# Kernel tuning notes

Hardware: AMD Instinct MI355X
Metric: run time of the kernel (lower is better)

Reference implementation:

```python
import jax, jax.numpy as jnp
import numpy as np

N_EMBED = 1024
HEAD_COUNT = 16
HEAD_SIZE = 64  # HEAD_COUNT * HEAD_SIZE == N_EMBED
SEQ = 2048
BATCH = 2


def setup_inputs() -> dict:
    key = jax.random.key(0)
    k_ix, k_q, k_k, k_v, k_p, k_b = jax.random.split(key, 6)
    scale = 1.0 / np.sqrt(N_EMBED)
    inp = {
        "ix": jax.random.normal(k_ix, (BATCH, SEQ, N_EMBED), dtype=jnp.float32),
        # per-head projection weights, stored as x @ W form: [H, C, D]
        "Wq": jax.random.normal(k_q, (HEAD_COUNT, N_EMBED, HEAD_SIZE), dtype=jnp.float32) * scale,
        "Wk": jax.random.normal(k_k, (HEAD_COUNT, N_EMBED, HEAD_SIZE), dtype=jnp.float32) * scale,
        "Wv": jax.random.normal(k_v, (HEAD_COUNT, N_EMBED, HEAD_SIZE), dtype=jnp.float32) * scale,
        # output projection (Linear with bias): y = x @ Wp + bp
        "Wp": jax.random.normal(k_p, (N_EMBED, N_EMBED), dtype=jnp.float32) * scale,
        "bp": jax.random.normal(k_b, (N_EMBED,), dtype=jnp.float32) * scale,
    }
    return inp


def reference(ix, Wq, Wk, Wv, Wp, bp):
    B, T, C = ix.shape
    # per-head projections: [B, H, T, D]
    Q = jnp.einsum("btc,hcd->bhtd", ix, Wq)
    K = jnp.einsum("btc,hcd->bhtd", ix, Wk)
    V = jnp.einsum("btc,hcd->bhtd", ix, Wv)
    # NOTE: faithful to source -- scores are MULTIPLIED by sqrt(C) (C = n_embed)
    scores = jnp.einsum("bhtd,bhsd->bhts", Q, K) * (C ** 0.5)
    causal = jnp.tril(jnp.ones((T, T), dtype=bool))
    scores = jnp.where(causal, scores, -jnp.inf)
    wei = jax.nn.softmax(scores, axis=-1)
    out = jnp.einsum("bhts,bhsd->bhtd", wei, V)
    # concat heads (matches torch.cat over per-head outputs along last dim)
    out = out.transpose(0, 2, 1, 3).reshape(B, T, -1)
    return out @ Wp + bp
```

## Files before the change

### kernel.cpp

```cpp
#include <hip/hip_runtime.h>

#define BATCH 2
#define SEQL  2048
#define NEMB  1024
#define NH    16
#define HD    64
#define MROWS (BATCH*SEQL)

typedef short bf16x8 __attribute__((ext_vector_type(8)));
typedef float f32x16 __attribute__((ext_vector_type(16)));

__device__ __forceinline__ unsigned short f2bf(float x) {
    union { float f; unsigned u; } v; v.f = x;
    unsigned r = v.u + 0x7FFFu + ((v.u >> 16) & 1u);
    return (unsigned short)(r >> 16);
}
__device__ __forceinline__ void split_bf16(float x, unsigned short& hi, unsigned short& lo) {
    hi = f2bf(x);
    union { unsigned u; float f; } h; h.u = ((unsigned)hi) << 16;
    lo = f2bf(x - h.f);
}

__device__ __forceinline__ int slot16(int chunk, int lane) {
    return chunk * 66 + (lane & 31) + 33 * (lane >> 5);
}

__global__ __launch_bounds__(256) void split_convert_kernel(
    const float* __restrict__ src,
    unsigned short* __restrict__ dhi, unsigned short* __restrict__ dlo)
{
    int i = (blockIdx.x * 256 + threadIdx.x) * 4;
    float4 v = *(const float4*)(src + i);
    unsigned short h[4], l[4];
    split_bf16(v.x, h[0], l[0]); split_bf16(v.y, h[1], l[1]);
    split_bf16(v.z, h[2], l[2]); split_bf16(v.w, h[3], l[3]);
    uint2 ph, pl;
    ph.x = h[0] | ((unsigned)h[1] << 16); ph.y = h[2] | ((unsigned)h[3] << 16);
    pl.x = l[0] | ((unsigned)l[1] << 16); pl.y = l[2] | ((unsigned)l[3] << 16);
    *(uint2*)(dhi + i) = ph;
    *(uint2*)(dlo + i) = pl;
}

__global__ __launch_bounds__(256) void transpose_convert_kernel(
    const float* __restrict__ Wq, const float* __restrict__ Wk,
    const float* __restrict__ Wv, const float* __restrict__ Wp,
    unsigned short* __restrict__ qhi, unsigned short* __restrict__ qlo,
    unsigned short* __restrict__ khi, unsigned short* __restrict__ klo,
    unsigned short* __restrict__ vhi, unsigned short* __restrict__ pt)
{
    __shared__ float tile[64][68];
    const int z = blockIdx.z, hb = blockIdx.y, c0 = blockIdx.x * 64;
    const float* src; int rstride; unsigned short* dhi; unsigned short* dlo;
    if (z == 0)      { src = Wq + (size_t)hb * 65536; rstride = 64;   dhi = qhi; dlo = qlo; }
    else if (z == 1) { src = Wk + (size_t)hb * 65536; rstride = 64;   dhi = khi; dlo = klo; }
    else if (z == 2) { src = Wv + (size_t)hb * 65536; rstride = 64;   dhi = vhi; dlo = nullptr; }
    else             { src = Wp + (size_t)hb * 64;    rstride = 1024; dhi = pt;  dlo = nullptr; }
    const int tid = threadIdx.x;
    #pragma unroll
    for (int i = 0; i < 4; ++i) {
        int fidx = i * 256 + tid;
        int r  = fidx >> 4;
        int dq = (fidx & 15) * 4;
        float4 v = *(const float4*)(src + (size_t)(c0 + r) * rstride + dq);
        *(float4*)&tile[r][dq] = v;
    }
    __syncthreads();
    #pragma unroll
    for (int i = 0; i < 4; ++i) {
        int fidx = i * 256 + tid;
        int d  = fidx >> 4;
        int cq = (fidx & 15) * 4;
        size_t base = (size_t)(hb * 64 + d) * 1024 + c0 + cq;
        unsigned short hh[4], ll[4];
        #pragma unroll
        for (int j = 0; j < 4; ++j) split_bf16(tile[cq + j][d], hh[j], ll[j]);
        uint2 ph; ph.x = hh[0] | ((unsigned)hh[1] << 16); ph.y = hh[2] | ((unsigned)hh[3] << 16);
        *(uint2*)(dhi + base) = ph;
        if (dlo) {
            uint2 pl; pl.x = ll[0] | ((unsigned)ll[1] << 16); pl.y = ll[2] | ((unsigned)ll[3] << 16);
            *(uint2*)(dlo + base) = pl;
        }
    }
}

__global__ __launch_bounds__(256) void qkv_gemm(
    const unsigned short* __restrict__ Ahi, const unsigned short* __restrict__ Alo,
    const unsigned short* __restrict__ Bq_hi, const unsigned short* __restrict__ Bq_lo,
    const unsigned short* __restrict__ Bk_hi, const unsigned short* __restrict__ Bk_lo,
    const unsigned short* __restrict__ Bv_hi,
    unsigned short* __restrict__ Qhi, unsigned short* __restrict__ Qlo,
    unsigned short* __restrict__ Khi, unsigned short* __restrict__ Klo,
    unsigned short* __restrict__ Vt)
{
    __shared__ unsigned short smem[16896];
    unsigned short* a_hi = smem;
    unsigned short* b_hi = smem + 4224;

    const int z = blockIdx.z;
    const bool split = (z < 2);
    const unsigned short* __restrict__ Bhi = (z == 0) ? Bq_hi : (z == 1) ? Bk_hi : Bv_hi;
    const unsigned short* __restrict__ Blo = (z == 0) ? Bq_lo : Bk_lo;
    unsigned short* __restrict__ Ohi = (z == 0) ? Qhi : Khi;
    unsigned short* __restrict__ Olo = (z == 0) ? Qlo : Klo;
    const float oscale = (z == 0) ? 32.0f : 1.0f;

    const int m0 = blockIdx.x * 128;
    const int n0 = blockIdx.y * 128;
    const int tid  = threadIdx.x;
    const int wid  = tid >> 6, lane = tid & 63;
    const int wr   = wid >> 1, wc = wid & 1;

    f32x16 acc[2][2] = {};

    for (int kk0 = 0; kk0 < NEMB; kk0 += 32) {
        __syncthreads();
        #pragma unroll
        for (int q = 0; q < 2; ++q) {
            int fidx = q * 256 + tid;
            int row  = fidx >> 2;
            int k8   = (fidx & 3) * 8;
            int chunk = (row >> 5) * 2 + (k8 >> 4);
            int lp    = (row & 31) + 32 * ((k8 >> 3) & 1);
            int slot  = slot16(chunk, lp) * 8;
            *(bf16x8*)(a_hi + slot) = *(const bf16x8*)(Ahi + (size_t)(m0 + row) * 1024 + kk0 + k8);
            *(bf16x8*)(b_hi + slot) = *(const bf16x8*)(Bhi + (size_t)(n0 + row) * 1024 + kk0 + k8);
            if (split) {
                *(bf16x8*)(smem + 8448  + slot) = *(const bf16x8*)(Alo + (size_t)(m0 + row) * 1024 + kk0 + k8);
                *(bf16x8*)(smem + 12672 + slot) = *(const bf16x8*)(Blo + (size_t)(n0 + row) * 1024 + kk0 + k8);
            }
        }
        __syncthreads();
        #pragma unroll
        for (int kch = 0; kch < 2; ++kch) {
            bf16x8 ah[2], bh_[2];
            #pragma unroll
            for (int mt = 0; mt < 2; ++mt)
                ah[mt] = *(const bf16x8*)(a_hi + slot16((2 * wr + mt) * 2 + kch, lane) * 8);
            #pragma unroll
            for (int nt = 0; nt < 2; ++nt)
                bh_[nt] = *(const bf16x8*)(b_hi + slot16((2 * wc + nt) * 2 + kch, lane) * 8);
            if (split) {
                bf16x8 al[2], bl[2];
                #pragma unroll
                for (int mt = 0; mt < 2; ++mt)
                    al[mt] = *(const bf16x8*)(smem + 8448 + slot16((2 * wr + mt) * 2 + kch, lane) * 8);
                #pragma unroll
                for (int nt = 0; nt < 2; ++nt)
                    bl[nt] = *(const bf16x8*)(smem + 12672 + slot16((2 * wc + nt) * 2 + kch, lane) * 8);
                #pragma unroll
                for (int mt = 0; mt < 2; ++mt)
                    #pragma unroll
                    for (int nt = 0; nt < 2; ++nt) {
                        acc[mt][nt] = __builtin_amdgcn_mfma_f32_32x32x16_bf16(ah[mt], bh_[nt], acc[mt][nt], 0, 0, 0);
                        acc[mt][nt] = __builtin_amdgcn_mfma_f32_32x32x16_bf16(ah[mt], bl[nt],  acc[mt][nt], 0, 0, 0);
                        acc[mt][nt] = __builtin_amdgcn_mfma_f32_32x32x16_bf16(al[mt], bh_[nt], acc[mt][nt], 0, 0, 0);
                    }
            } else {
                #pragma unroll
                for (int mt = 0; mt < 2; ++mt)
                    #pragma unroll
                    for (int nt = 0; nt < 2; ++nt)
                        acc[mt][nt] = __builtin_amdgcn_mfma_f32_32x32x16_bf16(bh_[nt], ah[mt], acc[mt][nt], 0, 0, 0);
            }
        }
    }

    #pragma unroll
    for (int mt = 0; mt < 2; ++mt) {
        #pragma unroll
        for (int nt = 0; nt < 2; ++nt) {
            if (z == 2) {
                const int mcol = m0 + wr * 64 + mt * 32 + (lane & 31);
                const int bb = mcol >> 11, tt = mcol & (SEQL - 1);
                #pragma unroll
                for (int r = 0; r < 16; ++r) {
                    int nrow = n0 + wc * 64 + nt * 32 + (r & 3) + 8 * (r >> 2) + 4 * (lane >> 5);
                    int head = nrow >> 6, dd = nrow & 63;
                    Vt[((size_t)(bb * NH + head) * HD + dd) * SEQL + tt] = f2bf(acc[mt][nt][r]);
                }
            } else {
                const int ncol = n0 + wc * 64 + nt * 32 + (lane & 31);
                const int head = ncol >> 6, d = ncol & 63;
                #pragma unroll
                for (int r = 0; r < 16; ++r) {
                    int mrow = m0 + wr * 64 + mt * 32 + (r & 3) + 8 * (r >> 2) + 4 * (lane >> 5);
                    int bb = mrow >> 11, t = mrow & (SEQL - 1);
                    size_t idx = ((size_t)(bb * NH + head) * SEQL + t) * HD + d;
                    float v = acc[mt][nt][r] * oscale;
                    unsigned short hi = f2bf(v);
                    Ohi[idx] = hi;
                    union { unsigned u; float f; } hf; hf.u = ((unsigned)hi) << 16;
                    Olo[idx] = f2bf(v - hf.f);
                }
            }
        }
    }
}

__global__ __launch_bounds__(256) void attn_mfma_kernel(
    const unsigned short* __restrict__ Qhi, const unsigned short* __restrict__ Qlo,
    const unsigned short* __restrict__ Khi, const unsigned short* __restrict__ Klo,
    const unsigned short* __restrict__ Vt,
    unsigned short* __restrict__ AO)
{
    __shared__ unsigned short smem[2][3][4224];

    const int bid = blockIdx.x;
    const int xcd = bid & 7;
    const int idx = bid >> 3;
    const int bh  = xcd * 4 + (idx & 3);
    const int g   = 15 - (idx >> 2);

    const int tid  = threadIdx.x;
    const int wid  = tid >> 6;
    const int lane = tid & 63;
    const int ln   = lane & 31;
    const int h    = lane >> 5;

    const int qb_idx = g * 4 + wid;
    const int qb     = qb_idx * 32;
    const int qglob  = qb + ln;
    const int my_nt  = (qb_idx >> 1) + 1;
    const int tmax   = 2 * g + 2;

    const unsigned short* __restrict__ Qbh = Qhi + (size_t)bh * SEQL * HD;
    const unsigned short* __restrict__ Qbl = Qlo + (size_t)bh * SEQL * HD;
    const unsigned short* __restrict__ Kbh = Khi + (size_t)bh * SEQL * HD;
    const unsigned short* __restrict__ Kbl = Klo + (size_t)bh * SEQL * HD;
    const unsigned short* __restrict__ Vtb = Vt  + (size_t)bh * HD * SEQL;

    bf16x8 qhi[4], qlo[4];
    #pragma unroll
    for (int c = 0; c < 4; ++c) {
        qhi[c] = *(const bf16x8*)(Qbh + (size_t)qglob * HD + c * 16 + h * 8);
        qlo[c] = *(const bf16x8*)(Qbl + (size_t)qglob * HD + c * 16 + h * 8);
    }

    int s_[2], d8_[2], ks_[2];
    #pragma unroll
    for (int ff = 0; ff < 2; ++ff) {
        int fidx = ff * 256 + tid;
        s_[ff]  = fidx >> 3;
        d8_[ff] = fidx & 7;
        ks_[ff] = slot16((s_[ff] >> 5) * 4 + (d8_[ff] >> 1),
                         (s_[ff] & 31) + 32 * (d8_[ff] & 1)) * 8;
    }

    bf16x8 kh[2], kl[2], vv[2];
    #pragma unroll
    for (int ff = 0; ff < 2; ++ff) {
        kh[ff] = *(const bf16x8*)(Kbh + (size_t)s_[ff] * HD + d8_[ff] * 8);
        kl[ff] = *(const bf16x8*)(Kbl + (size_t)s_[ff] * HD + d8_[ff] * 8);
        vv[ff] = *(const bf16x8*)(Vtb + (size_t)s_[ff] * SEQL + d8_[ff] * 8);
    }
    #pragma unroll
    for (int ff = 0; ff < 2; ++ff) {
        *(bf16x8*)(&smem[0][0][ks_[ff]]) = kh[ff];
        *(bf16x8*)(&smem[0][1][ks_[ff]]) = kl[ff];
        *(bf16x8*)(&smem[0][2][ks_[ff]]) = vv[ff];
    }
    if (tmax > 1) {
        #pragma unroll
        for (int ff = 0; ff < 2; ++ff) {
            kh[ff] = *(const bf16x8*)(Kbh + (size_t)(64 + s_[ff]) * HD + d8_[ff] * 8);
            kl[ff] = *(const bf16x8*)(Kbl + (size_t)(64 + s_[ff]) * HD + d8_[ff] * 8);
            vv[ff] = *(const bf16x8*)(Vtb + (size_t)s_[ff] * SEQL + 64 + d8_[ff] * 8);
        }
    }

    f32x16 oacc[2] = {};
    float m_run = -1e30f, l_run = 0.f;

    for (int t = 0; t < tmax; ++t) {
        __syncthreads();
        if (t + 1 < tmax) {
            const int nb = (t + 1) & 1;
            #pragma unroll
            for (int ff = 0; ff < 2; ++ff) {
                *(bf16x8*)(&smem[nb][0][ks_[ff]]) = kh[ff];
                *(bf16x8*)(&smem[nb][1][ks_[ff]]) = kl[ff];
                *(bf16x8*)(&smem[nb][2][ks_[ff]]) = vv[ff];
            }
            if (t + 2 < tmax) {
                const int s0n = (t + 2) * 64;
                #pragma unroll
                for (int ff = 0; ff < 2; ++ff) {
                    kh[ff] = *(const bf16x8*)(Kbh + (size_t)(s0n + s_[ff]) * HD + d8_[ff] * 8);
                    kl[ff] = *(const bf16x8*)(Kbl + (size_t)(s0n + s_[ff]) * HD + d8_[ff] * 8);
                    vv[ff] = *(const bf16x8*)(Vtb + (size_t)s_[ff] * SEQL + s0n + d8_[ff] * 8);
                }
            }
        }

        if (t < my_nt) {
            const int cb = t & 1;
            const int s0 = t * 64;
            const bf16x8* khf = (const bf16x8*)&smem[cb][0][0];
            const bf16x8* klf = (const bf16x8*)&smem[cb][1][0];
            const bf16x8* vtf = (const bf16x8*)&smem[cb][2][0];

            f32x16 sacc[2] = {};
            __builtin_amdgcn_s_setprio(1);
            #pragma unroll
            for (int sb = 0; sb < 2; ++sb) {
                #pragma unroll
                for (int c = 0; c < 4; ++c) {
                    bf16x8 ah = khf[slot16(sb * 4 + c, lane)];
                    bf16x8 al = klf[slot16(sb * 4 + c, lane)];
                    sacc[sb] = __builtin_amdgcn_mfma_f32_32x32x16_bf16(ah, qhi[c], sacc[sb], 0, 0, 0);
                    sacc[sb] = __builtin_amdgcn_mfma_f32_32x32x16_bf16(ah, qlo[c], sacc[sb], 0, 0, 0);
                    sacc[sb] = __builtin_amdgcn_mfma_f32_32x32x16_bf16(al, qhi[c], sacc[sb], 0, 0, 0);
                }
            }
            __builtin_amdgcn_s_setprio(0);

            const bool diag = (s0 + 63) > qb;
            float mtile = -1e30f;
            #pragma unroll
            for (int sb = 0; sb < 2; ++sb) {
                #pragma unroll
                for (int r = 0; r < 16; ++r) {
                    int srow = (r & 3) + 8 * (r >> 2) + 4 * h + sb * 32;
                    float x = sacc[sb][r];
                    if (diag && (s0 + srow) > qglob) x = -1e30f;
                    sacc[sb][r] = x;
                    mtile = fmaxf(mtile, x);
                }
            }
            mtile = fmaxf(mtile, __shfl_xor(mtile, 32));
            const float mnew  = fmaxf(m_run, mtile);
            const float alpha = __expf(m_run - mnew);

            float psum = 0.f;
            unsigned pw[2][8];
            #pragma unroll
            for (int sb = 0; sb < 2; ++sb) {
                #pragma unroll
                for (int r2 = 0; r2 < 8; ++r2) {
                    float p0 = __expf(sacc[sb][2 * r2]     - mnew);
                    float p1 = __expf(sacc[sb][2 * r2 + 1] - mnew);
                    psum += p0 + p1;
                    pw[sb][r2] = (unsigned)f2bf(p0) | ((unsigned)f2bf(p1) << 16);
                }
            }
            psum += __shfl_xor(psum, 32);
            l_run = l_run * alpha + psum;
            m_run = mnew;
            #pragma unroll
            for (int dt = 0; dt < 2; ++dt)
                #pragma unroll
                for (int r = 0; r < 16; ++r)
                    oacc[dt][r] *= alpha;

            unsigned px[2][8];
            #pragma unroll
            for (int sb = 0; sb < 2; ++sb)
                #pragma unroll
                for (int i = 0; i < 8; ++i)
                    px[sb][i] = __shfl_xor(pw[sb][i], 32);

            bf16x8 pfrag[4];
            #pragma unroll
            for (int sb = 0; sb < 2; ++sb) {
                #pragma unroll
                for (int c = 0; c < 2; ++c) {
                    unsigned u0, u1, u2, u3;
                    if (h == 0) { u0 = pw[sb][4*c];   u1 = pw[sb][4*c+1]; u2 = px[sb][4*c];   u3 = px[sb][4*c+1]; }
                    else        { u0 = px[sb][4*c+2]; u1 = px[sb][4*c+3]; u2 = pw[sb][4*c+2]; u3 = pw[sb][4*c+3]; }
                    union { unsigned u[4]; bf16x8 v; } cvt;
                    cvt.u[0] = u0; cvt.u[1] = u1; cvt.u[2] = u2; cvt.u[3] = u3;
                    pfrag[sb * 2 + c] = cvt.v;
                }
            }

            __builtin_amdgcn_s_setprio(1);
            #pragma unroll
            for (int dt = 0; dt < 2; ++dt)
                #pragma unroll
                for (int sc = 0; sc < 4; ++sc)
                    oacc[dt] = __builtin_amdgcn_mfma_f32_32x32x16_bf16(
                        vtf[slot16(dt * 4 + sc, lane)], pfrag[sc], oacc[dt], 0, 0, 0);
            __builtin_amdgcn_s_setprio(0);
        }
    }

    const float inv = 1.0f / l_run;
    unsigned short* aop = AO + ((size_t)(bh >> 4) * SEQL + qglob) * NEMB + (bh & 15) * HD;
    #pragma unroll
    for (int dt = 0; dt < 2; ++dt) {
        #pragma unroll
        for (int rg = 0; rg < 4; ++rg) {
            int d0 = dt * 32 + rg * 8 + h * 4;
            unsigned short b0 = f2bf(oacc[dt][rg * 4 + 0] * inv);
            unsigned short b1 = f2bf(oacc[dt][rg * 4 + 1] * inv);
            unsigned short b2 = f2bf(oacc[dt][rg * 4 + 2] * inv);
            unsigned short b3 = f2bf(oacc[dt][rg * 4 + 3] * inv);
            uint2 w;
            w.x = (unsigned)b0 | ((unsigned)b1 << 16);
            w.y = (unsigned)b2 | ((unsigned)b3 << 16);
            *(uint2*)(aop + d0) = w;
        }
    }
}

__global__ __launch_bounds__(256) void out_proj_kernel(
    const unsigned short* __restrict__ A, const unsigned short* __restrict__ B,
    const float* __restrict__ bias, float* __restrict__ out)
{
    __shared__ unsigned short smem[8448];
    unsigned short* a_s = smem;
    unsigned short* b_s = smem + 4224;

    const int m0 = blockIdx.x * 128;
    const int n0 = blockIdx.y * 128;
    const int tid  = threadIdx.x;
    const int wid  = tid >> 6, lane = tid & 63;
    const int wr   = wid >> 1, wc = wid & 1;

    f32x16 acc[2][2] = {};

    for (int kk0 = 0; kk0 < NEMB; kk0 += 32) {
        __syncthreads();
        #pragma unroll
        for (int q = 0; q < 2; ++q) {
            int fidx = q * 256 + tid;
            int row  = fidx >> 2;
            int k8   = (fidx & 3) * 8;
            int slot = slot16((row >> 5) * 2 + (k8 >> 4), (row & 31) + 32 * ((k8 >> 3) & 1)) * 8;
            *(bf16x8*)(a_s + slot) = *(const bf16x8*)(A + (size_t)(m0 + row) * 1024 + kk0 + k8);
            *(bf16x8*)(b_s + slot) = *(const bf16x8*)(B + (size_t)(n0 + row) * 1024 + kk0 + k8);
        }
        __syncthreads();
        #pragma unroll
        for (int kch = 0; kch < 2; ++kch) {
            bf16x8 ah[2], bh_[2];
            #pragma unroll
            for (int mt = 0; mt < 2; ++mt)
                ah[mt] = *(const bf16x8*)(a_s + slot16((2 * wr + mt) * 2 + kch, lane) * 8);
            #pragma unroll
            for (int nt = 0; nt < 2; ++nt)
                bh_[nt] = *(const bf16x8*)(b_s + slot16((2 * wc + nt) * 2 + kch, lane) * 8);
            #pragma unroll
            for (int mt = 0; mt < 2; ++mt)
                #pragma unroll
                for (int nt = 0; nt < 2; ++nt)
                    acc[mt][nt] = __builtin_amdgcn_mfma_f32_32x32x16_bf16(ah[mt], bh_[nt], acc[mt][nt], 0, 0, 0);
        }
    }

    #pragma unroll
    for (int mt = 0; mt < 2; ++mt) {
        #pragma unroll
        for (int nt = 0; nt < 2; ++nt) {
            const int ncol = n0 + wc * 64 + nt * 32 + (lane & 31);
            const float bv = bias[ncol];
            #pragma unroll
            for (int r = 0; r < 16; ++r) {
                int mrow = m0 + wr * 64 + mt * 32 + (r & 3) + 8 * (r >> 2) + 4 * (lane >> 5);
                out[(size_t)mrow * 1024 + ncol] = acc[mt][nt][r] + bv;
            }
        }
    }
}

extern "C" void kernel_launch(void* const* d_in, const int* in_sizes, int n_in,
                              void* d_out, int out_size, void* d_ws, size_t ws_size,
                              hipStream_t stream)
{
    const float* ix = (const float*)d_in[0];
    const float* Wq = (const float*)d_in[1];
    const float* Wk = (const float*)d_in[2];
    const float* Wv = (const float*)d_in[3];
    const float* Wp = (const float*)d_in[4];
    const float* bp = (const float*)d_in[5];
    float* out = (float*)d_out;

    char* ws = (char*)d_ws;
    #define WSOFF(mb) ((unsigned short*)(ws + (size_t)(mb) * 1024 * 1024))
    unsigned short* ix_hi  = WSOFF(0);
    unsigned short* ix_lo  = WSOFF(8);
    unsigned short* Wqt_hi = WSOFF(16);
    unsigned short* Wqt_lo = WSOFF(18);
    unsigned short* Wkt_hi = WSOFF(20);
    unsigned short* Wkt_lo = WSOFF(22);
    unsigned short* Wvt_hi = WSOFF(24);
    unsigned short* Qhi    = WSOFF(26);
    unsigned short* Qlo    = WSOFF(34);
    unsigned short* Khi    = WSOFF(42);
    unsigned short* Klo    = WSOFF(50);
    unsigned short* Wpt    = WSOFF(58);
    unsigned short* AObf   = WSOFF(0);
    unsigned short* Vt     = (unsigned short*)d_out;
    #undef WSOFF

    split_convert_kernel<<<MROWS * NEMB / 4 / 256, 256, 0, stream>>>(ix, ix_hi, ix_lo);
    transpose_convert_kernel<<<dim3(16, 16, 4), 256, 0, stream>>>(
        Wq, Wk, Wv, Wp, Wqt_hi, Wqt_lo, Wkt_hi, Wkt_lo, Wvt_hi, Wpt);
    qkv_gemm<<<dim3(MROWS / 128, NEMB / 128, 3), 256, 0, stream>>>(
        ix_hi, ix_lo, Wqt_hi, Wqt_lo, Wkt_hi, Wkt_lo, Wvt_hi,
        Qhi, Qlo, Khi, Klo, Vt);
    attn_mfma_kernel<<<512, 256, 0, stream>>>(Qhi, Qlo, Khi, Klo, Vt, AObf);
    out_proj_kernel<<<dim3(MROWS / 128, NEMB / 128), 256, 0, stream>>>(AObf, Wpt, bp, out);
}
```

Before: 206.3 us.

## Double-buffer LDS tiles with register prefetch in QKV and output GEMMs

Both the QKV projection GEMM and the output projection GEMM now use two LDS buffers. Each iteration writes the prefetched registers for tile t+1 into the alternate buffer and issues global loads for tile t+2 before running the MFMAs on tile t, which cuts one barrier per iteration and overlaps global latency with compute. Launch bounds now request 2 blocks per CU to cap register use. The cost is double the LDS footprint, about 67KB for qkv_gemm, which may limit occupancy, plus extra prefetch registers.

```diff
diff --git a/kernel.cpp b/kernel.cpp
--- a/kernel.cpp
+++ b/kernel.cpp
@@ -83,7 +83,7 @@
     }
 }
 
-__global__ __launch_bounds__(256) void qkv_gemm(
+__global__ __launch_bounds__(256, 2) void qkv_gemm(
     const unsigned short* __restrict__ Ahi, const unsigned short* __restrict__ Alo,
     const unsigned short* __restrict__ Bq_hi, const unsigned short* __restrict__ Bq_lo,
     const unsigned short* __restrict__ Bk_hi, const unsigned short* __restrict__ Bk_lo,
@@ -92,9 +92,7 @@
     unsigned short* __restrict__ Khi, unsigned short* __restrict__ Klo,
     unsigned short* __restrict__ Vt)
 {
-    __shared__ unsigned short smem[16896];
-    unsigned short* a_hi = smem;
-    unsigned short* b_hi = smem + 4224;
+    __shared__ unsigned short smem[2][4][4224];
 
     const int z = blockIdx.z;
     const bool split = (z < 2);
@@ -110,26 +108,60 @@
     const int wid  = tid >> 6, lane = tid & 63;
     const int wr   = wid >> 1, wc = wid & 1;
 
+    int roff_[2], slot_[2];
+    #pragma unroll
+    for (int q = 0; q < 2; ++q) {
+        int f   = q * 256 + tid;
+        int row = f >> 2;
+        int k8  = (f & 3) * 8;
+        roff_[q] = row * 1024 + k8;
+        slot_[q] = slot16((row >> 5) * 2 + (k8 >> 4), (row & 31) + 32 * ((k8 >> 3) & 1)) * 8;
+    }
+    const unsigned short* __restrict__ Ah = Ahi + (size_t)m0 * 1024;
+    const unsigned short* __restrict__ Bh = Bhi + (size_t)n0 * 1024;
+    const unsigned short* __restrict__ Al = split ? Alo + (size_t)m0 * 1024 : Ahi;
+    const unsigned short* __restrict__ Bl = split ? Blo + (size_t)n0 * 1024 : Bhi;
+
+    bf16x8 pah[2], pbh[2], pal[2], pbl[2];
+
+    #define LOADT(KK)  do { _Pragma("unroll")                                   \
+        for (int q = 0; q < 2; ++q) {                                           \
+            pah[q] = *(const bf16x8*)(Ah + roff_[q] + (KK));                    \
+            pbh[q] = *(const bf16x8*)(Bh + roff_[q] + (KK));                    \
+            if (split) {                                                        \
+                pal[q] = *(const bf16x8*)(Al + roff_[q] + (KK));                \
+                pbl[q] = *(const bf16x8*)(Bl + roff_[q] + (KK));                \
+            }                                                                   \
+        } } while (0)
+
+    #define WRITET(NB) do { _Pragma("unroll")                                   \
+        for (int q = 0; q < 2; ++q) {                                           \
+            *(bf16x8*)(&smem[NB][0][slot_[q]]) = pah[q];                        \
+            *(bf16x8*)(&smem[NB][1][slot_[q]]) = pbh[q];                        \
+            if (split) {                                                        \
+                *(bf16x8*)(&smem[NB][2][slot_[q]]) = pal[q];                    \
+                *(bf16x8*)(&smem[NB][3][slot_[q]]) = pbl[q];                    \
+            }                                                                   \
+        } } while (0)
+
     f32x16 acc[2][2] = {};
 
-    for (int kk0 = 0; kk0 < NEMB; kk0 += 32) {
+    LOADT(0);
+    WRITET(0);
+    LOADT(32);
+
+    for (int t = 0; t < 32; ++t) {
         __syncthreads();
-        #pragma unroll
-        for (int q = 0; q < 2; ++q) {
-            int fidx = q * 256 + tid;
-            int row  = fidx >> 2;
-            int k8   = (fidx & 3) * 8;
-            int chunk = (row >> 5) * 2 + (k8 >> 4);
-            int lp    = (row & 31) + 32 * ((k8 >> 3) & 1);
-            int slot  = slot16(chunk, lp) * 8;
-            *(bf16x8*)(a_hi + slot) = *(const bf16x8*)(Ahi + (size_t)(m0 + row) * 1024 + kk0 + k8);
-            *(bf16x8*)(b_hi + slot) = *(const bf16x8*)(Bhi + (size_t)(n0 + row) * 1024 + kk0 + k8);
-            if (split) {
-                *(bf16x8*)(smem + 8448  + slot) = *(const bf16x8*)(Alo + (size_t)(m0 + row) * 1024 + kk0 + k8);
-                *(bf16x8*)(smem + 12672 + slot) = *(const bf16x8*)(Blo + (size_t)(n0 + row) * 1024 + kk0 + k8);
-            }
-        }
-        __syncthreads();
+        if (t + 1 < 32) {
+            WRITET((t + 1) & 1);
+            if (t + 2 < 32) LOADT((t + 2) * 32);
+        }
+        const int cb = t & 1;
+        const unsigned short* a_hi = smem[cb][0];
+        const unsigned short* b_hi = smem[cb][1];
+        const unsigned short* a_lo = smem[cb][2];
+        const unsigned short* b_lo = smem[cb][3];
+
         #pragma unroll
         for (int kch = 0; kch < 2; ++kch) {
             bf16x8 ah[2], bh_[2];
@@ -143,10 +175,10 @@
                 bf16x8 al[2], bl[2];
                 #pragma unroll
                 for (int mt = 0; mt < 2; ++mt)
-                    al[mt] = *(const bf16x8*)(smem + 8448 + slot16((2 * wr + mt) * 2 + kch, lane) * 8);
+                    al[mt] = *(const bf16x8*)(a_lo + slot16((2 * wr + mt) * 2 + kch, lane) * 8);
                 #pragma unroll
                 for (int nt = 0; nt < 2; ++nt)
-                    bl[nt] = *(const bf16x8*)(smem + 12672 + slot16((2 * wc + nt) * 2 + kch, lane) * 8);
+                    bl[nt] = *(const bf16x8*)(b_lo + slot16((2 * wc + nt) * 2 + kch, lane) * 8);
                 #pragma unroll
                 for (int mt = 0; mt < 2; ++mt)
                     #pragma unroll
@@ -164,6 +196,8 @@
             }
         }
     }
+    #undef LOADT
+    #undef WRITET
 
     #pragma unroll
     for (int mt = 0; mt < 2; ++mt) {
@@ -403,13 +437,11 @@
     }
 }
 
-__global__ __launch_bounds__(256) void out_proj_kernel(
+__global__ __launch_bounds__(256, 2) void out_proj_kernel(
     const unsigned short* __restrict__ A, const unsigned short* __restrict__ B,
     const float* __restrict__ bias, float* __restrict__ out)
 {
-    __shared__ unsigned short smem[8448];
-    unsigned short* a_s = smem;
-    unsigned short* b_s = smem + 4224;
+    __shared__ unsigned short smem[2][2][4224];
 
     const int m0 = blockIdx.x * 128;
     const int n0 = blockIdx.y * 128;
@@ -417,20 +449,57 @@
     const int wid  = tid >> 6, lane = tid & 63;
     const int wr   = wid >> 1, wc = wid & 1;
 
+    int roff_[2], slot_[2];
+    #pragma unroll
+    for (int q = 0; q < 2; ++q) {
+        int f   = q * 256 + tid;
+        int row = f >> 2;
+        int k8  = (f & 3) * 8;
+        roff_[q] = row * 1024 + k8;
+        slot_[q] = slot16((row >> 5) * 2 + (k8 >> 4), (row & 31) + 32 * ((k8 >> 3) & 1)) * 8;
+    }
+    const unsigned short* __restrict__ Ab = A + (size_t)m0 * 1024;
+    const unsigned short* __restrict__ Bb = B + (size_t)n0 * 1024;
+
+    bf16x8 pa[2], pb[2];
+    #pragma unroll
+    for (int q = 0; q < 2; ++q) {
+        pa[q] = *(const bf16x8*)(Ab + roff_[q]);
+        pb[q] = *(const bf16x8*)(Bb + roff_[q]);
+    }
+    #pragma unroll
+    for (int q = 0; q < 2; ++q) {
+        *(bf16x8*)(&smem[0][0][slot_[q]]) = pa[q];
+        *(bf16x8*)(&smem[0][1][slot_[q]]) = pb[q];
+    }
+    #pragma unroll
+    for (int q = 0; q < 2; ++q) {
+        pa[q] = *(const bf16x8*)(Ab + roff_[q] + 32);
+        pb[q] = *(const bf16x8*)(Bb + roff_[q] + 32);
+    }
+
     f32x16 acc[2][2] = {};
 
-    for (int kk0 = 0; kk0 < NEMB; kk0 += 32) {
+    for (int t = 0; t < 32; ++t) {
         __syncthreads();
-        #pragma unroll
-        for (int q = 0; q < 2; ++q) {
-            int fidx = q * 256 + tid;
-            int row  = fidx >> 2;
-            int k8   = (fidx & 3) * 8;
-            int slot = slot16((row >> 5) * 2 + (k8 >> 4), (row & 31) + 32 * ((k8 >> 3) & 1)) * 8;
-            *(bf16x8*)(a_s + slot) = *(const bf16x8*)(A + (size_t)(m0 + row) * 1024 + kk0 + k8);
-            *(bf16x8*)(b_s + slot) = *(const bf16x8*)(B + (size_t)(n0 + row) * 1024 + kk0 + k8);
-        }
-        __syncthreads();
+        if (t + 1 < 32) {
+            const int nb = (t + 1) & 1;
+            #pragma unroll
+            for (int q = 0; q < 2; ++q) {
+                *(bf16x8*)(&smem[nb][0][slot_[q]]) = pa[q];
+                *(bf16x8*)(&smem[nb][1][slot_[q]]) = pb[q];
+            }
+            if (t + 2 < 32) {
+                #pragma unroll
+                for (int q = 0; q < 2; ++q) {
+                    pa[q] = *(const bf16x8*)(Ab + roff_[q] + (t + 2) * 32);
+                    pb[q] = *(const bf16x8*)(Bb + roff_[q] + (t + 2) * 32);
+                }
+            }
+        }
+        const int cb = t & 1;
+        const unsigned short* a_s = smem[cb][0];
+        const unsigned short* b_s = smem[cb][1];
         #pragma unroll
         for (int kch = 0; kch < 2; ++kch) {
             bf16x8 ah[2], bh_[2];
```

Result: faster. 193.4 us (-6.3%).
